# Optimization experiments

Measured on AMD Instinct MI355X. Metric: run time of the kernel, lower is better.

Reference implementation:

```python
import jax, jax.numpy as jnp
import numpy as np

DIM = 192
HEADS = 6
WS = 7          # window size
SHIFT = 3       # shift size
HID = 768       # mlp hidden
EPS = 1e-5


def _rel_pos_index(ws):
    coords = np.stack(np.meshgrid(np.arange(ws), np.arange(ws), indexing='ij'))  # (2, ws, ws)
    cf = coords.reshape(2, -1)                       # (2, ws*ws)
    rel = cf[:, :, None] - cf[:, None, :]            # (2, N, N)
    rel = rel.transpose(1, 2, 0).astype(np.int64)
    rel[:, :, 0] += ws - 1
    rel[:, :, 1] += ws - 1
    rel[:, :, 0] *= 2 * ws - 1
    return jnp.asarray(rel.sum(-1))                  # (N, N)

REL_IDX = _rel_pos_index(WS)


def _layernorm(x, w, b):
    mu = jnp.mean(x, axis=-1, keepdims=True)
    var = jnp.mean(jnp.square(x - mu), axis=-1, keepdims=True)
    return (x - mu) * jax.lax.rsqrt(var + EPS) * w + b


def setup_inputs() -> dict:
    key = jax.random.key(0)
    ks = jax.random.split(key, 8)
    B, H, W = 32, 56, 56
    s = 0.02
    return {
        'x': jax.random.normal(ks[0], (B, H * W, DIM), jnp.float32),
        'norm1_w': jnp.ones((DIM,), jnp.float32),
        'norm1_b': jnp.zeros((DIM,), jnp.float32),
        'qkv_w': jax.random.normal(ks[1], (3 * DIM, DIM), jnp.float32) * s,
        'qkv_b': jnp.zeros((3 * DIM,), jnp.float32),
        'rpb_table': jax.random.normal(ks[2], ((2 * WS - 1) ** 2, HEADS), jnp.float32) * s,
        'proj_w': jax.random.normal(ks[3], (DIM, DIM), jnp.float32) * s,
        'proj_b': jnp.zeros((DIM,), jnp.float32),
        'norm2_w': jnp.ones((DIM,), jnp.float32),
        'norm2_b': jnp.zeros((DIM,), jnp.float32),
        'fc1_w': jax.random.normal(ks[4], (HID, DIM), jnp.float32) * s,
        'fc1_b': jnp.zeros((HID,), jnp.float32),
        'fc2_w': jax.random.normal(ks[5], (DIM, HID), jnp.float32) * s,
        'fc2_b': jnp.zeros((DIM,), jnp.float32),
        'H': H,
        'W': W,
    }


def reference(x, norm1_w, norm1_b, qkv_w, qkv_b, rpb_table, proj_w, proj_b,
              norm2_w, norm2_b, fc1_w, fc1_b, fc2_w, fc2_b, H, W):
    B, L, C = x.shape
    d = C // HEADS
    scale = d ** -0.5
    N = WS * WS

    shortcut = x
    h = _layernorm(x, norm1_w, norm1_b).reshape(B, H, W, C)
    if SHIFT > 0:
        h = jnp.roll(h, shift=(-SHIFT, -SHIFT), axis=(1, 2))

    # window partition -> (B * nW, N, C)
    h = h.reshape(B, H // WS, WS, W // WS, WS, C).transpose(0, 1, 3, 2, 4, 5)
    hw = h.reshape(-1, N, C)

    # windowed attention (NOTE: the torch block never passes a shift mask)
    qkv = hw @ qkv_w.T + qkv_b                                    # (B_, N, 3C)
    qkv = qkv.reshape(-1, N, 3, HEADS, d).transpose(2, 0, 3, 1, 4)
    q, k, v = qkv[0] * scale, qkv[1], qkv[2]                      # (B_, h, N, d)
    attn = jnp.einsum('bhnd,bhmd->bhnm', q, k)
    bias = rpb_table[REL_IDX].transpose(2, 0, 1)                  # (h, N, N)
    attn = jax.nn.softmax(attn + bias[None], axis=-1)
    out = jnp.einsum('bhnm,bhmd->bhnd', attn, v)
    out = out.transpose(0, 2, 1, 3).reshape(-1, N, C)
    out = out @ proj_w.T + proj_b

    # window reverse -> (B, H, W, C)
    out = out.reshape(B, H // WS, W // WS, WS, WS, C).transpose(0, 1, 3, 2, 4, 5)
    out = out.reshape(B, H, W, C)
    if SHIFT > 0:
        out = jnp.roll(out, shift=(SHIFT, SHIFT), axis=(1, 2))

    x = shortcut + out.reshape(B, L, C)
    h2 = _layernorm(x, norm2_w, norm2_b)
    mlp = jax.nn.gelu(h2 @ fc1_w.T + fc1_b, approximate=False) @ fc2_w.T + fc2_b
    return x + mlp
```

## Files before the change

kernel.cpp:

```cpp
#include <hip/hip_runtime.h>
#include <hip/hip_bf16.h>
#include <cmath>

typedef float f32x4 __attribute__((ext_vector_type(4)));
typedef __bf16 bf16x8 __attribute__((ext_vector_type(8)));

#define WS_SZ 7
#define SHIFT 3
#define HGRID 56
#define C_DIM 192
#define NHEADS 6
#define HDIM 32
#define NTOK 100352
#define NWIN 2048

__device__ __forceinline__ int win_to_tok(int wrow) {
    int w = wrow / 49, i = wrow - w * 49;
    int b = w >> 6, rem = w & 63;
    int wy = rem >> 3, wx = rem & 7;
    int yi = i / 7, xi = i - yi * 7;
    int y = wy * 7 + yi + SHIFT; if (y >= HGRID) y -= HGRID;
    int x = wx * 7 + xi + SHIFT; if (x >= HGRID) x -= HGRID;
    return b * (HGRID * HGRID) + y * HGRID + x;
}

__global__ __launch_bounds__(256)
void cvt_kernel(const float* __restrict__ src, __bf16* __restrict__ dst, int n8)
{
    int idx = blockIdx.x * 256 + threadIdx.x;
    if (idx >= n8) return;
    float4 a = ((const float4*)src)[idx * 2];
    float4 b = ((const float4*)src)[idx * 2 + 1];
    bf16x8 o;
    o[0] = (__bf16)a.x; o[1] = (__bf16)a.y; o[2] = (__bf16)a.z; o[3] = (__bf16)a.w;
    o[4] = (__bf16)b.x; o[5] = (__bf16)b.y; o[6] = (__bf16)b.z; o[7] = (__bf16)b.w;
    ((bf16x8*)dst)[idx] = o;
}

__global__ __launch_bounds__(256)
void bias_expand_kernel(const float* __restrict__ rpb, float* __restrict__ bias_g)
{
    int idx = blockIdx.x * 256 + threadIdx.x;
    if (idx >= NHEADS * 2401) return;
    int h = idx / 2401, rem = idx - h * 2401;
    int i = rem / 49, j = rem - i * 49;
    int yi = i / 7, xi = i - yi * 7;
    int yj = j / 7, xj = j - yj * 7;
    int ri = (yi - yj + 6) * 13 + (xi - xj + 6);
    bias_g[idx] = rpb[ri * NHEADS + h];
}

template<int WINDOWED>
__global__ __launch_bounds__(256)
void ln_kernel(const float* __restrict__ x, const float* __restrict__ w,
               const float* __restrict__ b, __bf16* __restrict__ out)
{
    int r = blockIdx.x * 4 + (threadIdx.x >> 6);
    int lane = threadIdx.x & 63;
    int src = WINDOWED ? win_to_tok(r) : r;
    const float* xp = x + (size_t)src * C_DIM;
    float v0 = xp[lane], v1 = xp[lane + 64], v2 = xp[lane + 128];
    float s = v0 + v1 + v2;
    float sq = v0 * v0 + v1 * v1 + v2 * v2;
    #pragma unroll
    for (int off = 32; off; off >>= 1) {
        s  += __shfl_xor(s, off);
        sq += __shfl_xor(sq, off);
    }
    float mu = s * (1.f / C_DIM);
    float rs = rsqrtf(sq * (1.f / C_DIM) - mu * mu + 1e-5f);
    __bf16* op = out + (size_t)r * C_DIM;
    op[lane]       = (__bf16)((v0 - mu) * rs * w[lane]       + b[lane]);
    op[lane + 64]  = (__bf16)((v1 - mu) * rs * w[lane + 64]  + b[lane + 64]);
    op[lane + 128] = (__bf16)((v2 - mu) * rs * w[lane + 128] + b[lane + 128]);
}

template<int MODE>
__global__ __launch_bounds__(256)
void gemm_kernel(const __bf16* __restrict__ A, const __bf16* __restrict__ W,
                 const float* __restrict__ bias, void* __restrict__ outp,
                 const float* __restrict__ resid, int N, int K)
{
    __shared__ __bf16 As[128 * 40];
    __shared__ __bf16 Bs[64 * 40];
    const int tid = threadIdx.x;
    const int wave = tid >> 6, lane = tid & 63;
    const int wm = wave >> 1, wn = wave & 1;
    const int l15 = lane & 15, q8 = (lane >> 4) << 3;
    const int m0 = blockIdx.y * 128, n0 = blockIdx.x * 64;

    f32x4 acc[4][2];
    f32x4 zero = {0.f, 0.f, 0.f, 0.f};
    #pragma unroll
    for (int i = 0; i < 4; i++)
        #pragma unroll
        for (int j = 0; j < 2; j++) acc[i][j] = zero;

    const int br = tid >> 2, bc = (tid & 3) << 3;
    for (int kt = 0; kt < K; kt += 32) {
        __syncthreads();
        #pragma unroll
        for (int it = 0; it < 2; it++) {
            int idx = it * 256 + tid;
            int r = idx >> 2, c = (idx & 3) << 3;
            *(uint4*)(&As[r * 40 + c]) =
                *(const uint4*)(A + (size_t)(m0 + r) * K + kt + c);
        }
        *(uint4*)(&Bs[br * 40 + bc]) =
            *(const uint4*)(W + (size_t)(n0 + br) * K + kt + bc);
        __syncthreads();
        bf16x8 af[4], bfr[2];
        #pragma unroll
        for (int fm = 0; fm < 4; fm++)
            af[fm] = *(const bf16x8*)(&As[(wm * 64 + fm * 16 + l15) * 40 + q8]);
        #pragma unroll
        for (int fn = 0; fn < 2; fn++)
            bfr[fn] = *(const bf16x8*)(&Bs[(wn * 32 + fn * 16 + l15) * 40 + q8]);
        #pragma unroll
        for (int fm = 0; fm < 4; fm++)
            #pragma unroll
            for (int fn = 0; fn < 2; fn++)
                acc[fm][fn] = __builtin_amdgcn_mfma_f32_16x16x32_bf16(
                    af[fm], bfr[fn], acc[fm][fn], 0, 0, 0);
    }

    const int l4 = lane >> 4;
    #pragma unroll
    for (int fm = 0; fm < 4; fm++) {
        #pragma unroll
        for (int fn = 0; fn < 2; fn++) {
            int c = n0 + wn * 32 + fn * 16 + l15;
            float bv = bias[c];
            #pragma unroll
            for (int r = 0; r < 4; r++) {
                int m = m0 + wm * 64 + fm * 16 + l4 * 4 + r;
                float v = acc[fm][fn][r] + bv;
                if (MODE == 0) {
                    ((__bf16*)outp)[(size_t)m * N + c] = (__bf16)v;
                } else {
                    int t = win_to_tok(m);
                    ((float*)outp)[(size_t)t * C_DIM + c] =
                        resid[(size_t)t * C_DIM + c] + v;
                }
            }
        }
    }
}

__global__ __launch_bounds__(256, 3)
void mlp_fused_kernel(const float* __restrict__ n2w, const float* __restrict__ n2b,
                      const __bf16* __restrict__ w1,
                      const float* __restrict__ b1,
                      const __bf16* __restrict__ w2,
                      const float* __restrict__ b2,
                      float* __restrict__ out)
{
    __shared__ __align__(16) __bf16 As[64 * 200];
    __shared__ __bf16 Hs[64 * 72];
    const int tid = threadIdx.x;
    const int wn = tid >> 6, lane = tid & 63;
    const int l15 = lane & 15, q4 = lane >> 4, q8 = q4 << 3;
    const int m0 = blockIdx.x * 64;
    const int r0 = wn * 16;

    const __bf16* w1base = w1 + (size_t)(wn * 16 + l15) * 192 + q8;
    const __bf16* w2base = w2 + (size_t)(wn * 48 + l15) * 768 + q8;

    f32x4 zero = {0.f, 0.f, 0.f, 0.f};

    bf16x8 w1f[2][6];
    #pragma unroll
    for (int kt = 0; kt < 6; ++kt)
        w1f[0][kt] = *(const bf16x8*)(w1base + kt * 32);

    float bv1s[12];
    #pragma unroll
    for (int ch = 0; ch < 12; ++ch)
        bv1s[ch] = b1[ch * 64 + wn * 16 + l15];
    float bv2s[3];
    #pragma unroll
    for (int tn = 0; tn < 3; ++tn)
        bv2s[tn] = b2[wn * 48 + tn * 16 + l15];

    {
        const float wl0 = n2w[lane], wl1 = n2w[lane + 64], wl2 = n2w[lane + 128];
        const float bl0 = n2b[lane], bl1 = n2b[lane + 64], bl2 = n2b[lane + 128];
        #pragma unroll
        for (int rr = 0; rr < 16; ++rr) {
            const float* xp = out + (size_t)(m0 + r0 + rr) * C_DIM;
            float v0 = xp[lane], v1 = xp[lane + 64], v2 = xp[lane + 128];
            float s = v0 + v1 + v2;
            float sq = v0 * v0 + v1 * v1 + v2 * v2;
            #pragma unroll
            for (int off = 32; off; off >>= 1) {
                s  += __shfl_xor(s, off);
                sq += __shfl_xor(sq, off);
            }
            float mu = s * (1.f / C_DIM);
            float rs = rsqrtf(sq * (1.f / C_DIM) - mu * mu + 1e-5f);
            As[(r0 + rr) * 200 + lane]       = (__bf16)((v0 - mu) * rs * wl0 + bl0);
            As[(r0 + rr) * 200 + lane + 64]  = (__bf16)((v1 - mu) * rs * wl1 + bl1);
            As[(r0 + rr) * 200 + lane + 128] = (__bf16)((v2 - mu) * rs * wl2 + bl2);
        }
    }
    __syncthreads();

    f32x4 acc2[4][3];
    #pragma unroll
    for (int tm = 0; tm < 4; ++tm)
        #pragma unroll
        for (int tn = 0; tn < 3; ++tn) acc2[tm][tn] = zero;

    bf16x8 w2f[6];

    #pragma unroll
    for (int ch = 0; ch < 12; ++ch) {
        const int h0 = ch * 64;
        const int cur = ch & 1, nxt = cur ^ 1;

        if (ch < 11) {
            #pragma unroll
            for (int kt = 0; kt < 6; ++kt)
                w1f[nxt][kt] = *(const bf16x8*)(w1base + (size_t)(h0 + 64) * 192 + kt * 32);
        }
        #pragma unroll
        for (int ks = 0; ks < 2; ++ks)
            #pragma unroll
            for (int tn = 0; tn < 3; ++tn)
                w2f[ks * 3 + tn] = *(const bf16x8*)(w2base + (size_t)(tn * 16) * 768 + h0 + ks * 32);

        f32x4 acc1[4];
        #pragma unroll
        for (int tm = 0; tm < 4; ++tm) acc1[tm] = zero;
        #pragma unroll
        for (int kt = 0; kt < 6; ++kt)
            #pragma unroll
            for (int tm = 0; tm < 4; ++tm) {
                bf16x8 af = *(const bf16x8*)(&As[(tm * 16 + l15) * 200 + kt * 32 + q8]);
                acc1[tm] = __builtin_amdgcn_mfma_f32_16x16x32_bf16(
                    af, w1f[cur][kt], acc1[tm], 0, 0, 0);
            }

        __syncthreads();

        {
            const float bv = bv1s[ch];
            #pragma unroll
            for (int tm = 0; tm < 4; ++tm)
                #pragma unroll
                for (int r = 0; r < 4; ++r) {
                    int row = tm * 16 + q4 * 4 + r;
                    float v = acc1[tm][r] + bv;
                    float g = v * __builtin_amdgcn_rcpf(1.f + __expf(-1.702f * v));
                    Hs[row * 72 + wn * 16 + l15] = (__bf16)g;
                }
        }
        __syncthreads();

        #pragma unroll
        for (int ks = 0; ks < 2; ++ks)
            #pragma unroll
            for (int tm = 0; tm < 4; ++tm) {
                bf16x8 ap = *(const bf16x8*)(&Hs[(tm * 16 + l15) * 72 + ks * 32 + q8]);
                #pragma unroll
                for (int tn = 0; tn < 3; ++tn)
                    acc2[tm][tn] = __builtin_amdgcn_mfma_f32_16x16x32_bf16(
                        ap, w2f[ks * 3 + tn], acc2[tm][tn], 0, 0, 0);
            }
    }

    float* Cs = (float*)As;
    #pragma unroll
    for (int pass = 0; pass < 2; ++pass) {
        if (pass) __syncthreads();
        #pragma unroll
        for (int tmh = 0; tmh < 2; ++tmh) {
            int tm = pass * 2 + tmh;
            #pragma unroll
            for (int tn = 0; tn < 3; ++tn) {
                int c = wn * 48 + tn * 16 + l15;
                float bv = bv2s[tn];
                #pragma unroll
                for (int r = 0; r < 4; ++r) {
                    int rl = tmh * 16 + q4 * 4 + r;
                    Cs[rl * 196 + c] = acc2[tm][tn][r] + bv;
                }
            }
        }
        __syncthreads();
        #pragma unroll
        for (int it = 0; it < 6; ++it) {
            int f = it * 256 + tid;
            int row = f / 48, c4 = f - row * 48;
            float4* gp = (float4*)(out + (size_t)(m0 + pass * 32 + row) * C_DIM) + c4;
            float4 g = *gp;
            const float* lp = &Cs[row * 196 + c4 * 4];
            g.x += lp[0]; g.y += lp[1]; g.z += lp[2]; g.w += lp[3];
            *gp = g;
        }
    }
}

__global__ __launch_bounds__(256, 2)
void attn_mfma_kernel(const __bf16* __restrict__ qkv,
                      const float* __restrict__ bias_g,
                      __bf16* __restrict__ out)
{
    const int wave = threadIdx.x >> 6;
    const int lane = threadIdx.x & 63;
    const int pair = blockIdx.x * 4 + wave;
    const int w = pair / 6, head = pair - (pair / 6) * 6;

    __shared__ __bf16 vsT_s[4][32 * 72];
    __shared__ __bf16 Ps_s[4][64 * 72];
    __bf16* vsT = vsT_s[wave];
    __bf16* Ps  = Ps_s[wave];

    const int l15 = lane & 15, q4 = lane >> 4, q8 = q4 << 3;
    const size_t qbase = (size_t)w * 49 * 576 + head * 32;

    {
        int d = lane & 31, jh = lane >> 5;
        #pragma unroll
        for (int it = 0; it < 25; ++it) {
            int j = it * 2 + jh;
            if (j < 49)
                vsT[d * 72 + j] = qkv[qbase + (size_t)j * 576 + 384 + d];
        }
        for (int idx = lane; idx < 32 * 15; idx += 64) {
            int dd = idx / 15, jj = 49 + (idx - dd * 15);
            vsT[dd * 72 + jj] = (__bf16)0.f;
        }
    }

    bf16x8 qf[4], kf[4];
    #pragma unroll
    for (int t = 0; t < 4; ++t) {
        int row = t * 16 + l15;
        int rq = row < 49 ? row : 48;
        qf[t] = *(const bf16x8*)(qkv + qbase + (size_t)rq * 576 + q8);
        kf[t] = *(const bf16x8*)(qkv + qbase + (size_t)rq * 576 + 192 + q8);
    }

    f32x4 sc[4][4];
    f32x4 zero = {0.f, 0.f, 0.f, 0.f};
    #pragma unroll
    for (int tm = 0; tm < 4; ++tm)
        #pragma unroll
        for (int tn = 0; tn < 4; ++tn) sc[tm][tn] = zero;
    #pragma unroll
    for (int tm = 0; tm < 4; ++tm)
        #pragma unroll
        for (int tn = 0; tn < 4; ++tn)
            sc[tm][tn] = __builtin_amdgcn_mfma_f32_16x16x32_bf16(
                qf[tm], kf[tn], sc[tm][tn], 0, 0, 0);

    const float scale = 0.17677669529663687f;
    const int hbase = head * 2401;
    #pragma unroll
    for (int tm = 0; tm < 4; ++tm) {
        #pragma unroll
        for (int r = 0; r < 4; ++r) {
            int i = tm * 16 + q4 * 4 + r;
            int ioff = hbase + (i < 49 ? i : 48) * 49;
            float v[4];
            #pragma unroll
            for (int tn = 0; tn < 4; ++tn) {
                int j = tn * 16 + l15;
                float bz = (j < 49) ? bias_g[ioff + (j < 49 ? j : 0)] : 0.f;
                float t = sc[tm][tn][r] * scale + bz;
                v[tn] = (j < 49) ? t : -1e30f;
            }
            float mx = fmaxf(fmaxf(v[0], v[1]), fmaxf(v[2], v[3]));
            mx = fmaxf(mx, __shfl_xor(mx, 1));
            mx = fmaxf(mx, __shfl_xor(mx, 2));
            mx = fmaxf(mx, __shfl_xor(mx, 4));
            mx = fmaxf(mx, __shfl_xor(mx, 8));
            float sm = 0.f;
            #pragma unroll
            for (int tn = 0; tn < 4; ++tn) {
                float e = __expf(v[tn] - mx);
                sc[tm][tn][r] = e;
                sm += e;
            }
            sm += __shfl_xor(sm, 1);
            sm += __shfl_xor(sm, 2);
            sm += __shfl_xor(sm, 4);
            sm += __shfl_xor(sm, 8);
            float inv = __builtin_amdgcn_rcpf(sm);
            if (i < 49) {
                #pragma unroll
                for (int tn = 0; tn < 4; ++tn) {
                    int j = tn * 16 + l15;
                    Ps[i * 72 + j] = (__bf16)((j < 49) ? sc[tm][tn][r] * inv : 0.f);
                }
            }
        }
    }

    __syncthreads();

    f32x4 oc[4][2];
    #pragma unroll
    for (int tm = 0; tm < 4; ++tm)
        #pragma unroll
        for (int tn = 0; tn < 2; ++tn) oc[tm][tn] = zero;
    #pragma unroll
    for (int ks = 0; ks < 2; ++ks) {
        bf16x8 bv[2];
        #pragma unroll
        for (int tn = 0; tn < 2; ++tn)
            bv[tn] = *(const bf16x8*)(vsT + (tn * 16 + l15) * 72 + ks * 32 + q8);
        #pragma unroll
        for (int tm = 0; tm < 4; ++tm) {
            bf16x8 ap = *(const bf16x8*)(Ps + (tm * 16 + l15) * 72 + ks * 32 + q8);
            #pragma unroll
            for (int tn = 0; tn < 2; ++tn)
                oc[tm][tn] = __builtin_amdgcn_mfma_f32_16x16x32_bf16(
                    ap, bv[tn], oc[tm][tn], 0, 0, 0);
        }
    }

    #pragma unroll
    for (int tm = 0; tm < 4; ++tm) {
        #pragma unroll
        for (int r = 0; r < 4; ++r) {
            int m = tm * 16 + q4 * 4 + r;
            if (m < 49) {
                __bf16* op = out + (size_t)(w * 49 + m) * C_DIM + head * 32;
                #pragma unroll
                for (int tn = 0; tn < 2; ++tn)
                    op[tn * 16 + l15] = (__bf16)(oc[tm][tn][r]);
            }
        }
    }
}

extern "C" void kernel_launch(void* const* d_in, const int* in_sizes, int n_in,
                              void* d_out, int out_size, void* d_ws, size_t ws_size,
                              hipStream_t stream) {
    const float* x     = (const float*)d_in[0];
    const float* n1w   = (const float*)d_in[1];
    const float* n1b   = (const float*)d_in[2];
    const float* qkvw  = (const float*)d_in[3];
    const float* qkvb  = (const float*)d_in[4];
    const float* rpb   = (const float*)d_in[5];
    const float* projw = (const float*)d_in[6];
    const float* projb = (const float*)d_in[7];
    const float* n2w   = (const float*)d_in[8];
    const float* n2b   = (const float*)d_in[9];
    const float* fc1w  = (const float*)d_in[10];
    const float* fc1b  = (const float*)d_in[11];
    const float* fc2w  = (const float*)d_in[12];
    const float* fc2b  = (const float*)d_in[13];
    float* out = (float*)d_out;
    char* ws = (char*)d_ws;

    __bf16* bufA    = (__bf16*)ws;
    __bf16* bufQ    = (__bf16*)(ws + 38535168);
    __bf16* qkvw_b  = (__bf16*)(ws + 154140672);
    __bf16* projw_b = (__bf16*)(ws + 154361856);
    __bf16* fc1w_b  = (__bf16*)(ws + 154435584);
    __bf16* fc2w_b  = (__bf16*)(ws + 154730496);
    float*  bias_g  = (float*) (ws + 155025408);

    cvt_kernel<<<(110592/8 + 255)/256, 256, 0, stream>>>(qkvw, qkvw_b, 110592/8);
    cvt_kernel<<<(36864/8  + 255)/256, 256, 0, stream>>>(projw, projw_b, 36864/8);
    cvt_kernel<<<(147456/8 + 255)/256, 256, 0, stream>>>(fc1w, fc1w_b, 147456/8);
    cvt_kernel<<<(147456/8 + 255)/256, 256, 0, stream>>>(fc2w, fc2w_b, 147456/8);
    bias_expand_kernel<<<(NHEADS*2401 + 255)/256, 256, 0, stream>>>(rpb, bias_g);

    ln_kernel<1><<<NTOK / 4, 256, 0, stream>>>(x, n1w, n1b, bufA);
    gemm_kernel<0><<<dim3(9, NTOK / 128), 256, 0, stream>>>(
        bufA, qkvw_b, qkvb, bufQ, nullptr, 576, 192);
    attn_mfma_kernel<<<NWIN * NHEADS / 4, 256, 0, stream>>>(bufQ, bias_g, bufA);
    gemm_kernel<1><<<dim3(3, NTOK / 128), 256, 0, stream>>>(
        bufA, projw_b, projb, (void*)out, x, 192, 192);
    mlp_fused_kernel<<<NTOK / 64, 256, 0, stream>>>(
        n2w, n2b, fc1w_b, fc1b, fc2w_b, fc2b, out);
}
```

Baseline: 487.6 us.

## Transpose score MFMA so softmax rows sit in lanes, vectorize P stores

The QK^T MFMA now computes K·Q^T, so each lane holds four contiguous key columns of one query row. This cuts the softmax max and sum reductions from four cross-lane shuffles to two, makes the bias loads contiguous per lane, and lets probabilities be written to LDS as packed bf16x4 stores. It also drops the __syncthreads before the PV MFMA and wraps both MFMA phases in s_setprio. Removing the barrier is only safe if each block is a single wavefront. Since only the attention kernel changes, the effect on the whole block is bounded.

```diff
diff --git a/kernel.cpp b/kernel.cpp
--- a/kernel.cpp
+++ b/kernel.cpp
@@ -4,6 +4,7 @@
 
 typedef float f32x4 __attribute__((ext_vector_type(4)));
 typedef __bf16 bf16x8 __attribute__((ext_vector_type(8)));
+typedef __bf16 bf16x4 __attribute__((ext_vector_type(4)));
 
 #define WS_SZ 7
 #define SHIFT 3
@@ -345,60 +346,69 @@
     f32x4 sc[4][4];
     f32x4 zero = {0.f, 0.f, 0.f, 0.f};
     #pragma unroll
-    for (int tm = 0; tm < 4; ++tm)
-        #pragma unroll
-        for (int tn = 0; tn < 4; ++tn) sc[tm][tn] = zero;
-    #pragma unroll
-    for (int tm = 0; tm < 4; ++tm)
-        #pragma unroll
-        for (int tn = 0; tn < 4; ++tn)
-            sc[tm][tn] = __builtin_amdgcn_mfma_f32_16x16x32_bf16(
-                qf[tm], kf[tn], sc[tm][tn], 0, 0, 0);
+    for (int tn = 0; tn < 4; ++tn)
+        #pragma unroll
+        for (int tm = 0; tm < 4; ++tm) sc[tn][tm] = zero;
+    __builtin_amdgcn_s_setprio(1);
+    #pragma unroll
+    for (int tn = 0; tn < 4; ++tn)
+        #pragma unroll
+        for (int tm = 0; tm < 4; ++tm)
+            sc[tn][tm] = __builtin_amdgcn_mfma_f32_16x16x32_bf16(
+                kf[tn], qf[tm], sc[tn][tm], 0, 0, 0);
+    __builtin_amdgcn_s_setprio(0);
 
     const float scale = 0.17677669529663687f;
     const int hbase = head * 2401;
+    const int jb4 = q4 * 4;
     #pragma unroll
     for (int tm = 0; tm < 4; ++tm) {
-        #pragma unroll
-        for (int r = 0; r < 4; ++r) {
-            int i = tm * 16 + q4 * 4 + r;
-            int ioff = hbase + (i < 49 ? i : 48) * 49;
-            float v[4];
+        int i = tm * 16 + l15;
+        int ioff = hbase + (i < 49 ? i : 48) * 49;
+        float v[4][4];
+        #pragma unroll
+        for (int tn = 0; tn < 4; ++tn) {
+            int jb = tn * 16 + jb4;
+            #pragma unroll
+            for (int r = 0; r < 4; ++r) {
+                int j = jb + r;
+                float bz = (j < 49) ? bias_g[ioff + j] : 0.f;
+                float t = sc[tn][tm][r] * scale + bz;
+                v[tn][r] = (j < 49) ? t : -1e30f;
+            }
+        }
+        float mx = v[0][0];
+        #pragma unroll
+        for (int tn = 0; tn < 4; ++tn)
+            #pragma unroll
+            for (int r = 0; r < 4; ++r) mx = fmaxf(mx, v[tn][r]);
+        mx = fmaxf(mx, __shfl_xor(mx, 16));
+        mx = fmaxf(mx, __shfl_xor(mx, 32));
+        float sm = 0.f;
+        #pragma unroll
+        for (int tn = 0; tn < 4; ++tn)
+            #pragma unroll
+            for (int r = 0; r < 4; ++r) {
+                float e = __expf(v[tn][r] - mx);
+                v[tn][r] = e;
+                sm += e;
+            }
+        sm += __shfl_xor(sm, 16);
+        sm += __shfl_xor(sm, 32);
+        float inv = __builtin_amdgcn_rcpf(sm);
+        if (i < 49) {
             #pragma unroll
             for (int tn = 0; tn < 4; ++tn) {
-                int j = tn * 16 + l15;
-                float bz = (j < 49) ? bias_g[ioff + (j < 49 ? j : 0)] : 0.f;
-                float t = sc[tm][tn][r] * scale + bz;
-                v[tn] = (j < 49) ? t : -1e30f;
-            }
-            float mx = fmaxf(fmaxf(v[0], v[1]), fmaxf(v[2], v[3]));
-            mx = fmaxf(mx, __shfl_xor(mx, 1));
-            mx = fmaxf(mx, __shfl_xor(mx, 2));
-            mx = fmaxf(mx, __shfl_xor(mx, 4));
-            mx = fmaxf(mx, __shfl_xor(mx, 8));
-            float sm = 0.f;
-            #pragma unroll
-            for (int tn = 0; tn < 4; ++tn) {
-                float e = __expf(v[tn] - mx);
-                sc[tm][tn][r] = e;
-                sm += e;
-            }
-            sm += __shfl_xor(sm, 1);
-            sm += __shfl_xor(sm, 2);
-            sm += __shfl_xor(sm, 4);
-            sm += __shfl_xor(sm, 8);
-            float inv = __builtin_amdgcn_rcpf(sm);
-            if (i < 49) {
+                int jb = tn * 16 + jb4;
+                bf16x4 pk;
                 #pragma unroll
-                for (int tn = 0; tn < 4; ++tn) {
-                    int j = tn * 16 + l15;
-                    Ps[i * 72 + j] = (__bf16)((j < 49) ? sc[tm][tn][r] * inv : 0.f);
-                }
-            }
-        }
-    }
-
-    __syncthreads();
+                for (int r = 0; r < 4; ++r)
+                    pk[r] = (__bf16)((jb + r < 49) ? v[tn][r] * inv : 0.f);
+                *(bf16x4*)(&Ps[i * 72 + jb]) = pk;
+            }
+        }
+    }
+
 
     f32x4 oc[4][2];
     #pragma unroll
@@ -411,6 +421,7 @@
         #pragma unroll
         for (int tn = 0; tn < 2; ++tn)
             bv[tn] = *(const bf16x8*)(vsT + (tn * 16 + l15) * 72 + ks * 32 + q8);
+        __builtin_amdgcn_s_setprio(1);
         #pragma unroll
         for (int tm = 0; tm < 4; ++tm) {
             bf16x8 ap = *(const bf16x8*)(Ps + (tm * 16 + l15) * 72 + ks * 32 + q8);
@@ -419,6 +430,7 @@
                 oc[tm][tn] = __builtin_amdgcn_mfma_f32_16x16x32_bf16(
                     ap, bv[tn], oc[tm][tn], 0, 0, 0);
         }
+        __builtin_amdgcn_s_setprio(0);
     }
 
     #pragma unroll
```

Result: faster. 464.1 us (-4.8%).
